# Kernel optimization log

Hardware: AMD Instinct MI355X
Metric: run time of the kernel (lower is better)

## Reference

```python
import jax, jax.numpy as jnp
import numpy as np

N = 50000       # nodes
E = 800000      # edges (avg degree 16)
C_IN = 128
C_OUT = 128
H = 4           # attention heads
D = C_OUT // H  # per-head dim
G = 8           # group-norm groups
NEG_SLOPE_ACT = 0.01   # nn.LeakyReLU() default
NEG_SLOPE_ATT = 0.2    # GAT attention LeakyReLU slope


def _glorot(key, shape):
    fan = shape[0] + (shape[-1] if len(shape) > 1 else shape[0])
    lim = np.sqrt(6.0 / fan).astype(np.float32)
    return jax.random.uniform(key, shape, jnp.float32, -lim, lim)


def setup_inputs() -> dict:
    key = jax.random.key(0)
    ks = jax.random.split(key, 8)
    inp = {
        "x": jax.random.normal(ks[0], (N, C_IN), jnp.float32),
        "edge_index": jax.random.randint(ks[1], (2, E), 0, N),
        "edge_weight": jax.random.uniform(ks[2], (E,), jnp.float32),
    }
    dims = [C_IN, C_OUT]
    for l in range(2):
        cin = dims[l]
        k = jax.random.split(ks[3 + l], 8)
        inp[f"gamma{l}"] = jnp.ones((cin,), jnp.float32)
        inp[f"beta{l}"] = jnp.zeros((cin,), jnp.float32)
        inp[f"W{l}"] = _glorot(k[0], (cin, H * D))
        inp[f"We{l}"] = _glorot(k[1], (1, H * D))
        inp[f"a_src{l}"] = _glorot(k[2], (H, D))
        inp[f"a_dst{l}"] = _glorot(k[3], (H, D))
        inp[f"a_edge{l}"] = _glorot(k[4], (H, D))
        inp[f"bias{l}"] = jnp.zeros((H * D,), jnp.float32)
    return inp


def group_norm(x, gamma, beta, eps=1e-5):
    n, c = x.shape
    xg = x.reshape(n, G, c // G)
    mu = xg.mean(-1, keepdims=True)
    var = xg.var(-1, keepdims=True)
    xn = ((xg - mu) * jax.lax.rsqrt(var + eps)).reshape(n, c)
    return xn * gamma + beta


def gat_layer(x, src, dst, ew, W, We, a_src, a_dst, a_edge, bias):
    h = (x @ W).reshape(N, H, D)                   # [N,H,D]
    he = (ew[:, None] @ We).reshape(-1, H, D)      # [E',H,D] edge-weight embedding
    logits = ((h * a_src).sum(-1)[src]
              + (h * a_dst).sum(-1)[dst]
              + (he * a_edge).sum(-1))             # [E',H]
    logits = jax.nn.leaky_relu(logits, NEG_SLOPE_ATT)
    m = jax.ops.segment_max(logits, dst, num_segments=N)
    m = jax.lax.stop_gradient(jnp.where(jnp.isfinite(m), m, 0.0))
    e = jnp.exp(logits - m[dst])
    s = jax.ops.segment_sum(e, dst, num_segments=N)
    alpha = e / (s[dst] + 1e-16)                   # softmax over in-edges per dst, per head
    out = jax.ops.segment_sum(alpha[:, :, None] * h[src], dst, num_segments=N)
    return out.reshape(N, H * D) + bias


def reference(x, edge_index, edge_weight,
              gamma0, beta0, W0, We0, a_src0, a_dst0, a_edge0, bias0,
              gamma1, beta1, W1, We1, a_src1, a_dst1, a_edge1, bias1):
    loop = jnp.arange(N)
    src = jnp.concatenate([edge_index[0], loop])
    dst = jnp.concatenate([edge_index[1], loop])
    # self-loop fill_value='max': self edges get the max edge weight
    ew = jnp.concatenate([edge_weight, jnp.full((N,), edge_weight.max())])
    params = [(gamma0, beta0, W0, We0, a_src0, a_dst0, a_edge0, bias0),
              (gamma1, beta1, W1, We1, a_src1, a_dst1, a_edge1, bias1)]
    for g, b, W, We, asrc, adst, ae, bias in params:
        x = group_norm(x, g, b)
        x = jax.nn.leaky_relu(x, NEG_SLOPE_ACT)
        x = gat_layer(x, src, dst, ew, W, We, asrc, adst, ae, bias)
    return x
```

## Files before the change

### kernel.cpp

```cpp
#include <hip/hip_runtime.h>
#include <hip/hip_bf16.h>
#include <math.h>

#define CN 128
#define NBLK 128
#define BSH 8

typedef __attribute__((ext_vector_type(8))) short bf16x8;
typedef __attribute__((ext_vector_type(4))) float f32x4;

static __device__ inline unsigned int pack_bf16x2(float lo, float hi) {
    unsigned int ul = __float_as_uint(lo);
    unsigned int uh = __float_as_uint(hi);
    ul = (ul + 0x7fffu + ((ul >> 16) & 1u)) >> 16;
    uh = (uh + 0x7fffu + ((uh >> 16) & 1u)) & 0xffff0000u;
    return ul | uh;
}
static __device__ inline unsigned short bf16_of(float v) {
    unsigned int u = __float_as_uint(v);
    return (unsigned short)((u + 0x7fffu + ((u >> 16) & 1u)) >> 16);
}

__global__ __launch_bounds__(256) void kbA(const int* __restrict__ dsts,
                                           const float* __restrict__ ew,
                                           int e, int n,
                                           int* __restrict__ hist,
                                           int* __restrict__ ewmax,
                                           const float* __restrict__ W0,
                                           const float* __restrict__ W1,
                                           const float* __restrict__ We0,
                                           const float* __restrict__ ae0,
                                           const float* __restrict__ We1,
                                           const float* __restrict__ ae1,
                                           unsigned short* __restrict__ wt0,
                                           unsigned short* __restrict__ wt1,
                                           float* __restrict__ ce) {
    __shared__ int lh[256];
    int t = threadIdx.x, blk = blockIdx.x;
    if (blk >= NBLK) {
        int b = blk - NBLK;
        if (b < 2) {
            const float* W = b ? W1 : W0;
            unsigned short* wt = b ? wt1 : wt0;
            for (int i = t; i < CN * CN; i += 256) {
                int k = i >> 7, c = i & 127;
                wt[c * CN + k] = bf16_of(W[k * CN + c]);
            }
        } else if (t < 8) {
            const float* We = (t < 4) ? We0 : We1;
            const float* ae = (t < 4) ? ae0 : ae1;
            int h = t & 3;
            float s = 0.f;
            for (int d = 0; d < 32; d++) s += We[h * 32 + d] * ae[h * 32 + d];
            ce[t] = s;
        }
        return;
    }
    lh[t] = 0;
    __syncthreads();
    int tot = e + n;
    int chunk = (tot + NBLK - 1) / NBLK;
    int start = blk * chunk, end = min(start + chunk, tot);
    float m = 0.f;
    for (int i = start + t; i < end; i += 256) {
        int d;
        if (i < e) { d = dsts[i]; m = fmaxf(m, ew[i]); }
        else       { d = i - e; }
        atomicAdd(&lh[d >> BSH], 1);
    }
#pragma unroll
    for (int off = 1; off < 64; off <<= 1) m = fmaxf(m, __shfl_xor(m, off));
    if ((t & 63) == 0) atomicMax(ewmax, __float_as_int(m));
    __syncthreads();
    hist[t * NBLK + blk] = lh[t];
}

__global__ __launch_bounds__(256) void kscanL(int* __restrict__ a,
                                              int* __restrict__ bsum) {
    __shared__ int wsum[4];
    int t = threadIdx.x, blk = blockIdx.x;
    int idx = blk * 256 + t;
    int v = a[idx];
    int s = v;
    int lane = t & 63, wid = t >> 6;
#pragma unroll
    for (int off = 1; off < 64; off <<= 1) {
        int u = __shfl_up(s, off);
        if (lane >= off) s += u;
    }
    if (lane == 63) wsum[wid] = s;
    __syncthreads();
    int add = 0;
#pragma unroll
    for (int w = 0; w < 4; w++) if (w < wid) add += wsum[w];
    s += add;
    a[idx] = s - v;
    if (t == 255) bsum[blk] = s;
}

__global__ __launch_bounds__(128) void kscanS(int* __restrict__ bsum) {
    __shared__ int wtot;
    int t = threadIdx.x;
    int v = bsum[t];
    int s = v;
    int lane = t & 63, wid = t >> 6;
#pragma unroll
    for (int off = 1; off < 64; off <<= 1) {
        int u = __shfl_up(s, off);
        if (lane >= off) s += u;
    }
    if (t == 63) wtot = s;
    __syncthreads();
    if (wid == 1) s += wtot;
    bsum[t] = s - v;
}

__global__ __launch_bounds__(256) void kbB(const int* __restrict__ srcs,
                                           const int* __restrict__ dsts,
                                           const float* __restrict__ ew,
                                           const int* __restrict__ ewmax,
                                           const int* __restrict__ hsc,
                                           const int* __restrict__ bsum,
                                           int2* __restrict__ inter, int e, int n) {
    __shared__ int cur[256];
    int t = threadIdx.x, blk = blockIdx.x;
    cur[t] = hsc[t * NBLK + blk] + bsum[t >> 1];
    __syncthreads();
    int tot = e + n;
    float wmax = __int_as_float(*ewmax);
    int chunk = (tot + NBLK - 1) / NBLK;
    int start = blk * chunk, end = min(start + chunk, tot);
    for (int i = start + t; i < end; i += 256) {
        int s, d; float w;
        if (i < e) { s = srcs[i]; d = dsts[i]; w = ew[i]; }
        else       { s = i - e;   d = s;       w = wmax;  }
        int p = atomicAdd(&cur[d >> BSH], 1);
        inter[p] = make_int2((d << 16) | s, __float_as_int(w));
    }
}

__global__ __launch_bounds__(256) void kbC(const int* __restrict__ hsc,
                                           const int* __restrict__ bsum,
                                           const int2* __restrict__ inter,
                                           unsigned int* __restrict__ edges,
                                           int* __restrict__ rowptr,
                                           int n, int nb, int ep) {
    __shared__ int cnt[256];
    __shared__ int cur[256];
    __shared__ int wsum[4];
    int t = threadIdx.x, b = blockIdx.x;
    int rstart = hsc[b * NBLK] + bsum[b >> 1];
    int rend = (b + 1 < 256) ? (hsc[(b + 1) * NBLK] + bsum[(b + 1) >> 1]) : ep;
    cnt[t] = 0;
    __syncthreads();
    for (int i = rstart + t; i < rend; i += 256)
        atomicAdd(&cnt[(inter[i].x >> 16) & 255], 1);
    __syncthreads();
    int v = cnt[t];
    int s = v;
    int lane = t & 63, wid = t >> 6;
#pragma unroll
    for (int off = 1; off < 64; off <<= 1) {
        int u = __shfl_up(s, off);
        if (lane >= off) s += u;
    }
    if (lane == 63) wsum[wid] = s;
    __syncthreads();
    int wexcl = 0;
#pragma unroll
    for (int w = 0; w < 4; w++) if (w < wid) wexcl += wsum[w];
    int excl = wexcl + s - v;
    int node = (b << BSH) + t;
    int gpos = rstart + excl;
    if (node < n) rowptr[node] = gpos;
    if (b == nb - 1 && t == 0) rowptr[n] = ep;
    cur[t] = gpos;
    __syncthreads();
    for (int i = rstart + t; i < rend; i += 256) {
        int2 r = inter[i];
        int p = atomicAdd(&cur[(r.x >> 16) & 255], 1);
        unsigned int wb = bf16_of(__int_as_float(r.y));
        edges[p] = (unsigned int)(r.x & 0xffff) | (wb << 16);
    }
}

__global__ __launch_bounds__(256, 3) void kgn_gemm7(
        const float* __restrict__ xin, const uint4* __restrict__ xin_b,
        int inbf16, const float* __restrict__ gamma,
        const float* __restrict__ beta, const unsigned short* __restrict__ wt,
        const float* __restrict__ asrc, const float* __restrict__ adst,
        unsigned int* __restrict__ hout, float* __restrict__ ssrc,
        float* __restrict__ sdst, int n) {
    __shared__ short xs[64 * CN];
    __shared__ short ws[CN * CN];

    int t = threadIdx.x;
    int lane = t & 63, w = t >> 6;
    int m = lane & 15, quad = lane >> 4;
    int block_row = blockIdx.x * 64;

    {
        const uint4* src = (const uint4*)wt;
        uint4* dst = (uint4*)ws;
#pragma unroll
        for (int i = 0; i < 8; i++) {
            int u = t + 256 * i;
            int c = u >> 4, kb = u & 15;
            dst[c * 16 + (kb ^ (c & 15))] = src[u];
        }
    }
    {
        int r = t & 63;
        int row = block_row + r;
        uint4* dst = (uint4*)xs;
#pragma unroll
        for (int u2 = 0; u2 < 2; u2++) {
            int g = (t >> 6) * 2 + u2;
            uint4 lo, hi;
            if (row < n) {
                float v[16];
                if (inbf16) {
                    uint4 A = xin_b[(size_t)row * 16 + g * 2];
                    uint4 B = xin_b[(size_t)row * 16 + g * 2 + 1];
                    unsigned int uu[8] = {A.x,A.y,A.z,A.w,B.x,B.y,B.z,B.w};
#pragma unroll
                    for (int j = 0; j < 8; j++) {
                        v[2*j]   = __uint_as_float(uu[j] << 16);
                        v[2*j+1] = __uint_as_float(uu[j] & 0xffff0000u);
                    }
                } else {
                    const float4* xr = (const float4*)(xin + (size_t)row * CN + g * 16);
                    float4 A = xr[0], B = xr[1], C = xr[2], D = xr[3];
                    float tmp[16] = {A.x,A.y,A.z,A.w,B.x,B.y,B.z,B.w,
                                     C.x,C.y,C.z,C.w,D.x,D.y,D.z,D.w};
#pragma unroll
                    for (int j = 0; j < 16; j++) v[j] = tmp[j];
                }
                float mu = 0.f;
#pragma unroll
                for (int j = 0; j < 16; j++) mu += v[j];
                mu *= 0.0625f;
                float var = 0.f;
#pragma unroll
                for (int j = 0; j < 16; j++) { float d2 = v[j] - mu; var += d2 * d2; }
                var *= 0.0625f;
                float rsv = rsqrtf(var + 1e-5f);
                const float4* gp = (const float4*)(gamma + g * 16);
                const float4* bp = (const float4*)(beta + g * 16);
                float4 g0 = gp[0], g1 = gp[1], g2 = gp[2], g3 = gp[3];
                float4 b0 = bp[0], b1 = bp[1], b2 = bp[2], b3 = bp[3];
                float gv[16] = {g0.x,g0.y,g0.z,g0.w,g1.x,g1.y,g1.z,g1.w,
                                g2.x,g2.y,g2.z,g2.w,g3.x,g3.y,g3.z,g3.w};
                float bv[16] = {b0.x,b0.y,b0.z,b0.w,b1.x,b1.y,b1.z,b1.w,
                                b2.x,b2.y,b2.z,b2.w,b3.x,b3.y,b3.z,b3.w};
                float xn[16];
#pragma unroll
                for (int j = 0; j < 16; j++) {
                    float xv = (v[j] - mu) * rsv * gv[j] + bv[j];
                    xn[j] = xv > 0.f ? xv : 0.01f * xv;
                }
                lo = make_uint4(pack_bf16x2(xn[0], xn[1]),  pack_bf16x2(xn[2], xn[3]),
                                pack_bf16x2(xn[4], xn[5]),  pack_bf16x2(xn[6], xn[7]));
                hi = make_uint4(pack_bf16x2(xn[8], xn[9]),  pack_bf16x2(xn[10], xn[11]),
                                pack_bf16x2(xn[12], xn[13]), pack_bf16x2(xn[14], xn[15]));
            } else {
                lo = make_uint4(0, 0, 0, 0);
                hi = lo;
            }
            dst[r * 16 + ((2 * g)     ^ (r & 15))] = lo;
            dst[r * 16 + ((2 * g + 1) ^ (r & 15))] = hi;
        }
    }
    __syncthreads();

    f32x4 acc[4][2];
#pragma unroll
    for (int i = 0; i < 4; i++) { acc[i][0] = (f32x4)0.f; acc[i][1] = (f32x4)0.f; }

#pragma unroll
    for (int kc = 0; kc < 4; kc++) {
        int kb = 4 * kc + quad;
        bf16x8 af[4], bfr[2];
#pragma unroll
        for (int mt = 0; mt < 4; mt++)
            af[mt] = *(const bf16x8*)&xs[(16 * mt + m) * CN + ((kb ^ m) << 3)];
#pragma unroll
        for (int nt = 0; nt < 2; nt++) {
            int c = 32 * w + 16 * nt + m;
            bfr[nt] = *(const bf16x8*)&ws[c * CN + ((kb ^ m) << 3)];
        }
#pragma unroll
        for (int mt = 0; mt < 4; mt++) {
#pragma unroll
            for (int nt = 0; nt < 2; nt++)
                acc[mt][nt] = __builtin_amdgcn_mfma_f32_16x16x32_bf16(
                    af[mt], bfr[nt], acc[mt][nt], 0, 0, 0);
        }
    }

    float asv[2], adv[2];
#pragma unroll
    for (int nt = 0; nt < 2; nt++) {
        asv[nt] = asrc[32 * w + 16 * nt + m];
        adv[nt] = adst[32 * w + 16 * nt + m];
    }
#pragma unroll
    for (int mt = 0; mt < 4; mt++) {
#pragma unroll
        for (int j = 0; j < 4; j++) {
            float p = acc[mt][0][j] * asv[0] + acc[mt][1][j] * asv[1];
            float q = acc[mt][0][j] * adv[0] + acc[mt][1][j] * adv[1];
#pragma unroll
            for (int off = 1; off < 16; off <<= 1) {
                p += __shfl_xor(p, off);
                q += __shfl_xor(q, off);
            }
            if (m == 0) {
                int row = block_row + 16 * mt + 4 * quad + j;
                if (row < n) {
                    ssrc[row * 4 + w] = p;
                    sdst[row * 4 + w] = q;
                }
            }
        }
    }

    __syncthreads();
#pragma unroll
    for (int mt = 0; mt < 4; mt++) {
#pragma unroll
        for (int nt = 0; nt < 2; nt++) {
            int c = 32 * w + 16 * nt + m;
#pragma unroll
            for (int j = 0; j < 4; j++) {
                int rl = 16 * mt + 4 * quad + j;
                xs[rl * CN + c] = (short)bf16_of(acc[mt][nt][j]);
            }
        }
    }
    __syncthreads();
    {
        const uint4* src = (const uint4*)xs;
#pragma unroll
        for (int i = 0; i < 4; i++) {
            int u = t + 256 * i;
            int rl = u >> 4;
            int row = block_row + rl;
            if (row < n)
                *(uint4*)&hout[(size_t)row * 64 + ((u & 15) << 2)] = src[u];
        }
    }
}

__global__ __launch_bounds__(256, 8) void kaggr3(
        const uint4* __restrict__ h, const float* __restrict__ ssrc,
        const float* __restrict__ sdst, const int* __restrict__ rowptr,
        const unsigned int* __restrict__ edges, const float* __restrict__ ce4,
        const float* __restrict__ bias, float* __restrict__ out,
        uint4* __restrict__ outb, int packout, int n) {
    int t = threadIdx.x;
    int node = blockIdx.x * 4 + (t >> 6);
    if (node >= n) return;
    int l64 = t & 63;
    int ll = l64 & 15;
    int g  = l64 >> 4;
    int head = ll >> 2;

    int start = rowptr[node], end = rowptr[node + 1];
    float sd = sdst[node * 4 + head];
    float ce = ce4[head];

    float a0=0.f,a1=0.f,a2=0.f,a3=0.f,a4=0.f,a5=0.f,a6=0.f,a7=0.f;
    float se = 0.f;

    int i = start + g;
    for (; i + 12 < end; i += 16) {
        unsigned int er[4];
#pragma unroll
        for (int u = 0; u < 4; u++) er[u] = edges[i + 4 * u];
        float ssv[4]; uint4 U[4];
#pragma unroll
        for (int u = 0; u < 4; u++) {
            int sidx = er[u] & 0xffff;
            ssv[u] = ssrc[sidx * 4 + head];
            U[u] = h[(size_t)sidx * 16 + ll];
        }
#pragma unroll
        for (int u = 0; u < 4; u++) {
            float wv = __uint_as_float(er[u] & 0xffff0000u);
            float l = ssv[u] + sd + wv * ce;
            l = fmaxf(l, 0.2f * l);
            float e = __expf(fminf(l, 80.f));
            float h0 = __uint_as_float(U[u].x << 16);
            float h1 = __uint_as_float(U[u].x & 0xffff0000u);
            float h2 = __uint_as_float(U[u].y << 16);
            float h3 = __uint_as_float(U[u].y & 0xffff0000u);
            float h4 = __uint_as_float(U[u].z << 16);
            float h5 = __uint_as_float(U[u].z & 0xffff0000u);
            float h6 = __uint_as_float(U[u].w << 16);
            float h7 = __uint_as_float(U[u].w & 0xffff0000u);
            se += e;
            a0 = fmaf(e, h0, a0); a1 = fmaf(e, h1, a1);
            a2 = fmaf(e, h2, a2); a3 = fmaf(e, h3, a3);
            a4 = fmaf(e, h4, a4); a5 = fmaf(e, h5, a5);
            a6 = fmaf(e, h6, a6); a7 = fmaf(e, h7, a7);
        }
    }
    for (; i < end; i += 4) {
        unsigned int er = edges[i];
        int sidx = er & 0xffff;
        float ss = ssrc[sidx * 4 + head];
        uint4 U = h[(size_t)sidx * 16 + ll];
        float wv = __uint_as_float(er & 0xffff0000u);
        float l = ss + sd + wv * ce;
        l = fmaxf(l, 0.2f * l);
        float e = __expf(fminf(l, 80.f));
        float h0 = __uint_as_float(U.x << 16);
        float h1 = __uint_as_float(U.x & 0xffff0000u);
        float h2 = __uint_as_float(U.y << 16);
        float h3 = __uint_as_float(U.y & 0xffff0000u);
        float h4 = __uint_as_float(U.z << 16);
        float h5 = __uint_as_float(U.z & 0xffff0000u);
        float h6 = __uint_as_float(U.w << 16);
        float h7 = __uint_as_float(U.w & 0xffff0000u);
        se += e;
        a0 = fmaf(e, h0, a0); a1 = fmaf(e, h1, a1);
        a2 = fmaf(e, h2, a2); a3 = fmaf(e, h3, a3);
        a4 = fmaf(e, h4, a4); a5 = fmaf(e, h5, a5);
        a6 = fmaf(e, h6, a6); a7 = fmaf(e, h7, a7);
    }
#pragma unroll
    for (int off = 16; off < 64; off <<= 1) {
        a0 += __shfl_xor(a0, off); a1 += __shfl_xor(a1, off);
        a2 += __shfl_xor(a2, off); a3 += __shfl_xor(a3, off);
        a4 += __shfl_xor(a4, off); a5 += __shfl_xor(a5, off);
        a6 += __shfl_xor(a6, off); a7 += __shfl_xor(a7, off);
        se += __shfl_xor(se, off);
    }
    if (g == 0) {
        float inv = 1.f / (se + 1e-16f);
        const float4* bp = (const float4*)(bias + ll * 8);
        float4 b0 = bp[0], b1 = bp[1];
        float o0 = a0 * inv + b0.x, o1 = a1 * inv + b0.y;
        float o2 = a2 * inv + b0.z, o3 = a3 * inv + b0.w;
        float o4 = a4 * inv + b1.x, o5 = a5 * inv + b1.y;
        float o6 = a6 * inv + b1.z, o7 = a7 * inv + b1.w;
        if (packout) {
            outb[(size_t)node * 16 + ll] =
                make_uint4(pack_bf16x2(o0, o1), pack_bf16x2(o2, o3),
                           pack_bf16x2(o4, o5), pack_bf16x2(o6, o7));
        } else {
            float4* orow = (float4*)(out + (size_t)node * CN + ll * 8);
            orow[0] = make_float4(o0, o1, o2, o3);
            orow[1] = make_float4(o4, o5, o6, o7);
        }
    }
}

extern "C" void kernel_launch(void* const* d_in, const int* in_sizes, int n_in,
                              void* d_out, int out_size, void* d_ws, size_t ws_size,
                              hipStream_t stream) {
    const float* x  = (const float*)d_in[0];
    const int*   ei = (const int*)d_in[1];
    const float* ew = (const float*)d_in[2];
    int N_ = in_sizes[0] / CN;
    int E_ = in_sizes[2];
    int EP = E_ + N_;
    int NB = (N_ + 255) >> BSH;

    size_t off = 0;
    auto alloc = [&](size_t bytes) -> void* {
        void* p = (char*)d_ws + off;
        off += (bytes + 255) & ~(size_t)255;
        return p;
    };
    unsigned int* hbuf = (unsigned int*)alloc((size_t)N_ * 64 * 4);
    uint4* x1b     = (uint4*)alloc((size_t)N_ * 64 * 4);
    float* ssrc    = (float*)alloc((size_t)N_ * 4 * 4);
    float* sdst    = (float*)alloc((size_t)N_ * 4 * 4);
    int*   rowptr  = (int*)alloc((size_t)(N_ + 1) * 4);
    unsigned int* edges = (unsigned int*)alloc((size_t)EP * 4);
    int2*  inter   = (int2*)alloc((size_t)EP * 8);
    int*   hist    = (int*)alloc((size_t)256 * NBLK * 4);
    int*   bsum    = (int*)alloc(1024);
    int*   ewmax   = (int*)alloc(256);
    unsigned short* wt0 = (unsigned short*)alloc((size_t)CN * CN * 2);
    unsigned short* wt1 = (unsigned short*)alloc((size_t)CN * CN * 2);
    float* cedge   = (float*)alloc(256);

    hipMemsetAsync(ewmax, 0, 4, stream);

    const int* srcs = ei;
    const int* dsts = ei + E_;

    kbA<<<NBLK + 3, 256, 0, stream>>>(dsts, ew, E_, N_, hist, ewmax,
                                      (const float*)d_in[5], (const float*)d_in[13],
                                      (const float*)d_in[6], (const float*)d_in[9],
                                      (const float*)d_in[14], (const float*)d_in[17],
                                      wt0, wt1, cedge);
    kscanL<<<NBLK, 256, 0, stream>>>(hist, bsum);
    kscanS<<<1, 128, 0, stream>>>(bsum);
    kbB<<<NBLK, 256, 0, stream>>>(srcs, dsts, ew, ewmax, hist, bsum, inter, E_, N_);
    kbC<<<NB, 256, 0, stream>>>(hist, bsum, inter, edges, rowptr, N_, NB, EP);

    for (int l = 0; l < 2; l++) {
        const float* gamma = (const float*)d_in[3 + l * 8 + 0];
        const float* beta  = (const float*)d_in[3 + l * 8 + 1];
        const float* asrc  = (const float*)d_in[3 + l * 8 + 4];
        const float* adst  = (const float*)d_in[3 + l * 8 + 5];
        const float* bias  = (const float*)d_in[3 + l * 8 + 7];
        const unsigned short* wt = (l == 0) ? wt0 : wt1;

        kgn_gemm7<<<(N_ + 63) / 64, 256, 0, stream>>>(
            x, (const uint4*)x1b, l, gamma, beta, wt, asrc, adst,
            hbuf, ssrc, sdst, N_);
        kaggr3<<<(N_ + 3) / 4, 256, 0, stream>>>(
            (const uint4*)hbuf, ssrc, sdst, rowptr, edges, cedge + l * 4,
            bias, (float*)d_out, x1b, (l == 0) ? 1 : 0, N_);
    }
}
```

Baseline: 269.1 us.

## Replace two-pass bucketed CSR build with direct global-atomic counting sort

The CSR construction used to run as a coarse bucket histogram, a scatter into an int2 intermediate and a per-bucket local sort. It now counts in-degree per node with global atomics, scans the counts, and scatters edges straight to their final slots using a second global atomic per edge. This removes one kernel launch and the intermediate buffer's extra read and write traffic, at the cost of heavily contended global atomics and an extra memset. Edge order within each node's list becomes nondeterministic, which can change floating-point summation order.

```diff
diff --git a/kernel.cpp b/kernel.cpp
--- a/kernel.cpp
+++ b/kernel.cpp
@@ -3,8 +3,7 @@
 #include <math.h>
 
 #define CN 128
-#define NBLK 128
-#define BSH 8
+#define GRID_P 512
 
 typedef __attribute__((ext_vector_type(8))) short bf16x8;
 typedef __attribute__((ext_vector_type(4))) float f32x4;
@@ -21,24 +20,23 @@
     return (unsigned short)((u + 0x7fffu + ((u >> 16) & 1u)) >> 16);
 }
 
-__global__ __launch_bounds__(256) void kbA(const int* __restrict__ dsts,
-                                           const float* __restrict__ ew,
-                                           int e, int n,
-                                           int* __restrict__ hist,
-                                           int* __restrict__ ewmax,
-                                           const float* __restrict__ W0,
-                                           const float* __restrict__ W1,
-                                           const float* __restrict__ We0,
-                                           const float* __restrict__ ae0,
-                                           const float* __restrict__ We1,
-                                           const float* __restrict__ ae1,
-                                           unsigned short* __restrict__ wt0,
-                                           unsigned short* __restrict__ wt1,
-                                           float* __restrict__ ce) {
-    __shared__ int lh[256];
+__global__ __launch_bounds__(256) void kcount(const int* __restrict__ dsts,
+                                              const float* __restrict__ ew,
+                                              int e, int n,
+                                              int* __restrict__ cnt,
+                                              int* __restrict__ ewmax,
+                                              const float* __restrict__ W0,
+                                              const float* __restrict__ W1,
+                                              const float* __restrict__ We0,
+                                              const float* __restrict__ ae0,
+                                              const float* __restrict__ We1,
+                                              const float* __restrict__ ae1,
+                                              unsigned short* __restrict__ wt0,
+                                              unsigned short* __restrict__ wt1,
+                                              float* __restrict__ ce) {
     int t = threadIdx.x, blk = blockIdx.x;
-    if (blk >= NBLK) {
-        int b = blk - NBLK;
+    if (blk >= GRID_P) {
+        int b = blk - GRID_P;
         if (b < 2) {
             const float* W = b ? W1 : W0;
             unsigned short* wt = b ? wt1 : wt0;
@@ -56,31 +54,26 @@
         }
         return;
     }
-    lh[t] = 0;
-    __syncthreads();
     int tot = e + n;
-    int chunk = (tot + NBLK - 1) / NBLK;
-    int start = blk * chunk, end = min(start + chunk, tot);
     float m = 0.f;
-    for (int i = start + t; i < end; i += 256) {
+    for (int i = blk * 256 + t; i < tot; i += GRID_P * 256) {
         int d;
         if (i < e) { d = dsts[i]; m = fmaxf(m, ew[i]); }
         else       { d = i - e; }
-        atomicAdd(&lh[d >> BSH], 1);
+        atomicAdd(&cnt[d], 1);
     }
 #pragma unroll
     for (int off = 1; off < 64; off <<= 1) m = fmaxf(m, __shfl_xor(m, off));
     if ((t & 63) == 0) atomicMax(ewmax, __float_as_int(m));
-    __syncthreads();
-    hist[t * NBLK + blk] = lh[t];
-}
-
-__global__ __launch_bounds__(256) void kscanL(int* __restrict__ a,
+}
+
+__global__ __launch_bounds__(256) void kscanA(int* __restrict__ cnt,
+                                              int* __restrict__ rowptrL,
                                               int* __restrict__ bsum) {
     __shared__ int wsum[4];
     int t = threadIdx.x, blk = blockIdx.x;
     int idx = blk * 256 + t;
-    int v = a[idx];
+    int v = cnt[idx];
     int s = v;
     int lane = t & 63, wid = t >> 6;
 #pragma unroll
@@ -94,14 +87,15 @@
 #pragma unroll
     for (int w = 0; w < 4; w++) if (w < wid) add += wsum[w];
     s += add;
-    a[idx] = s - v;
+    rowptrL[idx] = s - v;
+    cnt[idx] = 0;
     if (t == 255) bsum[blk] = s;
 }
 
-__global__ __launch_bounds__(128) void kscanS(int* __restrict__ bsum) {
-    __shared__ int wtot;
+__global__ __launch_bounds__(256) void kscanB(int* __restrict__ bsum, int nb) {
+    __shared__ int wsum[4];
     int t = threadIdx.x;
-    int v = bsum[t];
+    int v = (t < nb) ? bsum[t] : 0;
     int s = v;
     int lane = t & 63, wid = t >> 6;
 #pragma unroll
@@ -109,78 +103,39 @@
         int u = __shfl_up(s, off);
         if (lane >= off) s += u;
     }
-    if (t == 63) wtot = s;
+    if (lane == 63) wsum[wid] = s;
     __syncthreads();
-    if (wid == 1) s += wtot;
+    int add = 0;
+#pragma unroll
+    for (int w = 0; w < 4; w++) if (w < wid) add += wsum[w];
+    s += add;
     bsum[t] = s - v;
 }
 
-__global__ __launch_bounds__(256) void kbB(const int* __restrict__ srcs,
-                                           const int* __restrict__ dsts,
-                                           const float* __restrict__ ew,
-                                           const int* __restrict__ ewmax,
-                                           const int* __restrict__ hsc,
-                                           const int* __restrict__ bsum,
-                                           int2* __restrict__ inter, int e, int n) {
-    __shared__ int cur[256];
+__global__ __launch_bounds__(256) void kscatter(const int* __restrict__ srcs,
+                                                const int* __restrict__ dsts,
+                                                const float* __restrict__ ew,
+                                                const int* __restrict__ ewmax,
+                                                const int* __restrict__ rowptrL,
+                                                const int* __restrict__ bsum,
+                                                int* __restrict__ cnt,
+                                                int* __restrict__ rowptr,
+                                                unsigned int* __restrict__ edges,
+                                                int e, int n) {
     int t = threadIdx.x, blk = blockIdx.x;
-    cur[t] = hsc[t * NBLK + blk] + bsum[t >> 1];
-    __syncthreads();
+    int gid = blk * 256 + t;
+    int stride = GRID_P * 256;
+    for (int i = gid; i < n; i += stride)
+        rowptr[i] = rowptrL[i] + bsum[i >> 8];
+    if (gid == 0) rowptr[n] = e + n;
     int tot = e + n;
     float wmax = __int_as_float(*ewmax);
-    int chunk = (tot + NBLK - 1) / NBLK;
-    int start = blk * chunk, end = min(start + chunk, tot);
-    for (int i = start + t; i < end; i += 256) {
+    for (int i = gid; i < tot; i += stride) {
         int s, d; float w;
         if (i < e) { s = srcs[i]; d = dsts[i]; w = ew[i]; }
         else       { s = i - e;   d = s;       w = wmax;  }
-        int p = atomicAdd(&cur[d >> BSH], 1);
-        inter[p] = make_int2((d << 16) | s, __float_as_int(w));
-    }
-}
-
-__global__ __launch_bounds__(256) void kbC(const int* __restrict__ hsc,
-                                           const int* __restrict__ bsum,
-                                           const int2* __restrict__ inter,
-                                           unsigned int* __restrict__ edges,
-                                           int* __restrict__ rowptr,
-                                           int n, int nb, int ep) {
-    __shared__ int cnt[256];
-    __shared__ int cur[256];
-    __shared__ int wsum[4];
-    int t = threadIdx.x, b = blockIdx.x;
-    int rstart = hsc[b * NBLK] + bsum[b >> 1];
-    int rend = (b + 1 < 256) ? (hsc[(b + 1) * NBLK] + bsum[(b + 1) >> 1]) : ep;
-    cnt[t] = 0;
-    __syncthreads();
-    for (int i = rstart + t; i < rend; i += 256)
-        atomicAdd(&cnt[(inter[i].x >> 16) & 255], 1);
-    __syncthreads();
-    int v = cnt[t];
-    int s = v;
-    int lane = t & 63, wid = t >> 6;
-#pragma unroll
-    for (int off = 1; off < 64; off <<= 1) {
-        int u = __shfl_up(s, off);
-        if (lane >= off) s += u;
-    }
-    if (lane == 63) wsum[wid] = s;
-    __syncthreads();
-    int wexcl = 0;
-#pragma unroll
-    for (int w = 0; w < 4; w++) if (w < wid) wexcl += wsum[w];
-    int excl = wexcl + s - v;
-    int node = (b << BSH) + t;
-    int gpos = rstart + excl;
-    if (node < n) rowptr[node] = gpos;
-    if (b == nb - 1 && t == 0) rowptr[n] = ep;
-    cur[t] = gpos;
-    __syncthreads();
-    for (int i = rstart + t; i < rend; i += 256) {
-        int2 r = inter[i];
-        int p = atomicAdd(&cur[(r.x >> 16) & 255], 1);
-        unsigned int wb = bf16_of(__int_as_float(r.y));
-        edges[p] = (unsigned int)(r.x & 0xffff) | (wb << 16);
+        int p = rowptrL[d] + bsum[d >> 8] + atomicAdd(&cnt[d], 1);
+        edges[p] = (unsigned int)(s & 0xffff) | ((unsigned int)bf16_of(w) << 16);
     }
 }
 
@@ -466,7 +421,7 @@
     int N_ = in_sizes[0] / CN;
     int E_ = in_sizes[2];
     int EP = E_ + N_;
-    int NB = (N_ + 255) >> BSH;
+    int NB = (N_ + 255) >> 8;
 
     size_t off = 0;
     auto alloc = [&](size_t bytes) -> void* {
@@ -480,8 +435,8 @@
     float* sdst    = (float*)alloc((size_t)N_ * 4 * 4);
     int*   rowptr  = (int*)alloc((size_t)(N_ + 1) * 4);
     unsigned int* edges = (unsigned int*)alloc((size_t)EP * 4);
-    int2*  inter   = (int2*)alloc((size_t)EP * 8);
-    int*   hist    = (int*)alloc((size_t)256 * NBLK * 4);
+    int*   cnt     = (int*)alloc((size_t)NB * 256 * 4);
+    int*   rowptrL = (int*)alloc((size_t)NB * 256 * 4);
     int*   bsum    = (int*)alloc(1024);
     int*   ewmax   = (int*)alloc(256);
     unsigned short* wt0 = (unsigned short*)alloc((size_t)CN * CN * 2);
@@ -489,19 +444,20 @@
     float* cedge   = (float*)alloc(256);
 
     hipMemsetAsync(ewmax, 0, 4, stream);
+    hipMemsetAsync(cnt, 0, (size_t)NB * 256 * 4, stream);
 
     const int* srcs = ei;
     const int* dsts = ei + E_;
 
-    kbA<<<NBLK + 3, 256, 0, stream>>>(dsts, ew, E_, N_, hist, ewmax,
-                                      (const float*)d_in[5], (const float*)d_in[13],
-                                      (const float*)d_in[6], (const float*)d_in[9],
-                                      (const float*)d_in[14], (const float*)d_in[17],
-                                      wt0, wt1, cedge);
-    kscanL<<<NBLK, 256, 0, stream>>>(hist, bsum);
-    kscanS<<<1, 128, 0, stream>>>(bsum);
-    kbB<<<NBLK, 256, 0, stream>>>(srcs, dsts, ew, ewmax, hist, bsum, inter, E_, N_);
-    kbC<<<NB, 256, 0, stream>>>(hist, bsum, inter, edges, rowptr, N_, NB, EP);
+    kcount<<<GRID_P + 3, 256, 0, stream>>>(dsts, ew, E_, N_, cnt, ewmax,
+                                           (const float*)d_in[5], (const float*)d_in[13],
+                                           (const float*)d_in[6], (const float*)d_in[9],
+                                           (const float*)d_in[14], (const float*)d_in[17],
+                                           wt0, wt1, cedge);
+    kscanA<<<NB, 256, 0, stream>>>(cnt, rowptrL, bsum);
+    kscanB<<<1, 256, 0, stream>>>(bsum, NB);
+    kscatter<<<GRID_P, 256, 0, stream>>>(srcs, dsts, ew, ewmax, rowptrL, bsum,
+                                         cnt, rowptr, edges, E_, N_);
 
     for (int l = 0; l < 2; l++) {
         const float* gamma = (const float*)d_in[3 + l * 8 + 0];
```

Measured after the change: 331.7 us. 23.3% more time.

## Fold block-sum scan and edge-weight max into consumers, drop memset and scan launch

Applied to the files above, without the earlier changes.

Doubles the number of CSR-build blocks to 256 and removes the separate single-block scan kernel. The block-sum scan is now recomputed redundantly inside each kbB and kbC block. The global atomicMax plus memset for the max edge weight is replaced by per-block partial maxima that kbB reduces itself. This cuts two small launches and a memset from the serial preprocessing chain, at the cost of redundant scan work per block and a larger histogram.

```diff
diff --git a/kernel.cpp b/kernel.cpp
--- a/kernel.cpp
+++ b/kernel.cpp
@@ -3,7 +3,7 @@
 #include <math.h>
 
 #define CN 128
-#define NBLK 128
+#define NBLK 256
 #define BSH 8
 
 typedef __attribute__((ext_vector_type(8))) short bf16x8;
@@ -25,7 +25,7 @@
                                            const float* __restrict__ ew,
                                            int e, int n,
                                            int* __restrict__ hist,
-                                           int* __restrict__ ewmax,
+                                           int* __restrict__ ewmaxArr,
                                            const float* __restrict__ W0,
                                            const float* __restrict__ W1,
                                            const float* __restrict__ We0,
@@ -36,6 +36,7 @@
                                            unsigned short* __restrict__ wt1,
                                            float* __restrict__ ce) {
     __shared__ int lh[256];
+    __shared__ int wm[4];
     int t = threadIdx.x, blk = blockIdx.x;
     if (blk >= NBLK) {
         int b = blk - NBLK;
@@ -70,9 +71,11 @@
     }
 #pragma unroll
     for (int off = 1; off < 64; off <<= 1) m = fmaxf(m, __shfl_xor(m, off));
-    if ((t & 63) == 0) atomicMax(ewmax, __float_as_int(m));
+    if ((t & 63) == 0) wm[t >> 6] = __float_as_int(m);
     __syncthreads();
     hist[t * NBLK + blk] = lh[t];
+    if (t == 0)
+        ewmaxArr[blk] = max(max(wm[0], wm[1]), max(wm[2], wm[3]));
 }
 
 __global__ __launch_bounds__(256) void kscanL(int* __restrict__ a,
@@ -98,44 +101,48 @@
     if (t == 255) bsum[blk] = s;
 }
 
-__global__ __launch_bounds__(128) void kscanS(int* __restrict__ bsum) {
-    __shared__ int wtot;
-    int t = threadIdx.x;
-    int v = bsum[t];
-    int s = v;
-    int lane = t & 63, wid = t >> 6;
-#pragma unroll
-    for (int off = 1; off < 64; off <<= 1) {
-        int u = __shfl_up(s, off);
-        if (lane >= off) s += u;
-    }
-    if (t == 63) wtot = s;
-    __syncthreads();
-    if (wid == 1) s += wtot;
-    bsum[t] = s - v;
-}
-
 __global__ __launch_bounds__(256) void kbB(const int* __restrict__ srcs,
                                            const int* __restrict__ dsts,
                                            const float* __restrict__ ew,
-                                           const int* __restrict__ ewmax,
+                                           const int* __restrict__ ewmaxArr,
                                            const int* __restrict__ hsc,
                                            const int* __restrict__ bsum,
                                            int2* __restrict__ inter, int e, int n) {
     __shared__ int cur[256];
+    __shared__ int wsum[4];
+    __shared__ int wmI;
     int t = threadIdx.x, blk = blockIdx.x;
-    cur[t] = hsc[t * NBLK + blk] + bsum[t >> 1];
-    __syncthreads();
+    if (t == 0) wmI = 0;
+    int v = bsum[t];
+    int s = v;
+    int lane = t & 63, wid = t >> 6;
+#pragma unroll
+    for (int off = 1; off < 64; off <<= 1) {
+        int u = __shfl_up(s, off);
+        if (lane >= off) s += u;
+    }
+    int mi = ewmaxArr[t];
+#pragma unroll
+    for (int off = 1; off < 64; off <<= 1) mi = max(mi, __shfl_xor(mi, off));
+    if (lane == 63) wsum[wid] = s;
+    __syncthreads();
+    int add = 0;
+#pragma unroll
+    for (int w = 0; w < 4; w++) if (w < wid) add += wsum[w];
+    s += add;
+    cur[t] = hsc[t * NBLK + blk] + (s - v);
+    if (lane == 0) atomicMax(&wmI, mi);
+    __syncthreads();
+    float wmax = __int_as_float(wmI);
     int tot = e + n;
-    float wmax = __int_as_float(*ewmax);
     int chunk = (tot + NBLK - 1) / NBLK;
     int start = blk * chunk, end = min(start + chunk, tot);
     for (int i = start + t; i < end; i += 256) {
-        int s, d; float w;
-        if (i < e) { s = srcs[i]; d = dsts[i]; w = ew[i]; }
-        else       { s = i - e;   d = s;       w = wmax;  }
+        int sn, d; float w;
+        if (i < e) { sn = srcs[i]; d = dsts[i]; w = ew[i]; }
+        else       { sn = i - e;   d = sn;      w = wmax;  }
         int p = atomicAdd(&cur[d >> BSH], 1);
-        inter[p] = make_int2((d << 16) | s, __float_as_int(w));
+        inter[p] = make_int2((d << 16) | sn, __float_as_int(w));
     }
 }
 
@@ -148,17 +155,35 @@
     __shared__ int cnt[256];
     __shared__ int cur[256];
     __shared__ int wsum[4];
+    __shared__ int bexc[257];
     int t = threadIdx.x, b = blockIdx.x;
-    int rstart = hsc[b * NBLK] + bsum[b >> 1];
-    int rend = (b + 1 < 256) ? (hsc[(b + 1) * NBLK] + bsum[(b + 1) >> 1]) : ep;
+    int lane = t & 63, wid = t >> 6;
+    {
+        int v = bsum[t];
+        int s = v;
+#pragma unroll
+        for (int off = 1; off < 64; off <<= 1) {
+            int u = __shfl_up(s, off);
+            if (lane >= off) s += u;
+        }
+        if (lane == 63) wsum[wid] = s;
+        __syncthreads();
+        int add = 0;
+#pragma unroll
+        for (int w = 0; w < 4; w++) if (w < wid) add += wsum[w];
+        s += add;
+        bexc[t] = s - v;
+        if (t == 255) bexc[256] = s;
+    }
     cnt[t] = 0;
     __syncthreads();
+    int rstart = hsc[b * NBLK] + bexc[b];
+    int rend = (b + 1 < 256) ? (hsc[(b + 1) * NBLK] + bexc[b + 1]) : ep;
     for (int i = rstart + t; i < rend; i += 256)
         atomicAdd(&cnt[(inter[i].x >> 16) & 255], 1);
     __syncthreads();
     int v = cnt[t];
     int s = v;
-    int lane = t & 63, wid = t >> 6;
 #pragma unroll
     for (int off = 1; off < 64; off <<= 1) {
         int u = __shfl_up(s, off);
@@ -483,24 +508,21 @@
     int2*  inter   = (int2*)alloc((size_t)EP * 8);
     int*   hist    = (int*)alloc((size_t)256 * NBLK * 4);
     int*   bsum    = (int*)alloc(1024);
-    int*   ewmax   = (int*)alloc(256);
+    int*   ewmaxArr= (int*)alloc((size_t)NBLK * 4);
     unsigned short* wt0 = (unsigned short*)alloc((size_t)CN * CN * 2);
     unsigned short* wt1 = (unsigned short*)alloc((size_t)CN * CN * 2);
     float* cedge   = (float*)alloc(256);
 
-    hipMemsetAsync(ewmax, 0, 4, stream);
-
     const int* srcs = ei;
     const int* dsts = ei + E_;
 
-    kbA<<<NBLK + 3, 256, 0, stream>>>(dsts, ew, E_, N_, hist, ewmax,
+    kbA<<<NBLK + 3, 256, 0, stream>>>(dsts, ew, E_, N_, hist, ewmaxArr,
                                       (const float*)d_in[5], (const float*)d_in[13],
                                       (const float*)d_in[6], (const float*)d_in[9],
                                       (const float*)d_in[14], (const float*)d_in[17],
                                       wt0, wt1, cedge);
-    kscanL<<<NBLK, 256, 0, stream>>>(hist, bsum);
-    kscanS<<<1, 128, 0, stream>>>(bsum);
-    kbB<<<NBLK, 256, 0, stream>>>(srcs, dsts, ew, ewmax, hist, bsum, inter, E_, N_);
+    kscanL<<<256, 256, 0, stream>>>(hist, bsum);
+    kbB<<<NBLK, 256, 0, stream>>>(srcs, dsts, ew, ewmaxArr, hist, bsum, inter, E_, N_);
     kbC<<<NB, 256, 0, stream>>>(hist, bsum, inter, edges, rowptr, N_, NB, EP);
 
     for (int l = 0; l < 2; l++) {
```

Result: faster. 260.3 us (-3.3%).
